# Kernel tuning notes

Hardware: AMD Instinct MI355X
Metric: run time of the kernel (lower is better)

The kernel has to match this reference:

```python
import jax, jax.numpy as jnp
import numpy as np

EPS = 1e-06


def setup_inputs() -> dict:
    key = jax.random.key(0)
    k1, k2 = jax.random.split(key)
    x = jax.random.normal(k1, (16, 64, 256, 256), dtype=jnp.float32)
    gamma = jax.random.normal(k2, (1,), dtype=jnp.float32)
    return {"x": x, "gamma": gamma}


def reference(x, gamma):
    B, C, H, W = x.shape
    N = H * W
    v = x.reshape(B, C, N)                      # Q = K = V = flattened x
    # l2_norm: normalize across channel dim (dim=-2) per spatial position
    inv_norm = 1.0 / (jnp.linalg.norm(v, axis=1) + 1e-06)   # [B, N]
    qn = v * inv_norm[:, None, :]               # [B, C, N], Q and K normalized identically
    q_sum = jnp.sum(qn, axis=1)                 # [B, N] (sum over channels)
    # tailor_sum: 1 / (N + K^T-summed-Q + eps) -> [B, C]
    tailor = 1.0 / (N + jnp.einsum('bcn,bn->bc', qn, q_sum) + EPS)
    value_sum = jnp.sum(v, axis=1)[:, None, :]  # [B, 1, N], broadcasts over C
    matrix = jnp.einsum('bcn,bmn->bcm', v, qn)  # V @ K^T : [B, C, C]
    matrix_sum = value_sum + jnp.einsum('bcm,bmn->bcn', matrix, qn)  # [B, C, N]
    weight_value = matrix_sum * tailor[:, :, None]
    return x + gamma * weight_value.reshape(B, C, H, W)
```

## Files before the change

kernel.cpp:

```cpp
#include <hip/hip_runtime.h>
#include <stdint.h>

#define BATCH 16
#define CDIM 64
#define NDIM 65536
#define EPSV 1e-6f

typedef __attribute__((ext_vector_type(8))) _Float16 f16x8;
typedef __attribute__((ext_vector_type(4))) float f32x4;
typedef __attribute__((ext_vector_type(4))) uint32_t u32x4;
typedef __attribute__((ext_vector_type(4))) short s16x4;

static __device__ __forceinline__ short h2s(_Float16 h) {
    return (short)__builtin_bit_cast(unsigned short, h);
}
static __device__ __forceinline__ _Float16 s2h(short s) {
    return __builtin_bit_cast(_Float16, (unsigned short)s);
}

#define T1 256
#define P1 264
#define CHUNKS 4
#define NTILE1 64

__global__ __launch_bounds__(256, 4)
void gram_kernel(const float* __restrict__ x, float* __restrict__ pmat,
                 float* __restrict__ pt, short* __restrict__ ut,
                 float2* __restrict__ meta) {
    __shared__ __align__(16) short ldsU[CDIM][P1];
    __shared__ __align__(16) float ldsG[T1];
    __shared__ float red[4][CDIM];

    const int tid = threadIdx.x;
    const int b = blockIdx.x >> 6;
    const int tileIdx = blockIdx.x & 63;
    const int w = tid >> 6;
    const int lane = tid & 63;
    const int cq = lane >> 4;
    const int cr = lane & 15;

    f32x4 acc0 = {0.f, 0.f, 0.f, 0.f};
    f32x4 acc1 = acc0, acc2 = acc0, acc3 = acc0;
    float tpart = 0.f;

    const float* xbase = x + (size_t)b * CDIM * NDIM;

    for (int chunk = 0; chunk < CHUNKS; ++chunk) {
        const int n0 = tileIdx * (T1 * CHUNKS) + chunk * T1;
        const int n = n0 + tid;
        const float* xb = xbase + n;
        float ss = 0.f, cs = 0.f;
#pragma unroll 8
        for (int c = 0; c < CDIM; ++c) {
            float v = __builtin_nontemporal_load(xb + (size_t)c * NDIM);
            ss += v * v;
            cs += v;
            ldsU[c][tid] = h2s((_Float16)v);
        }
        const float inv = 1.f / (sqrtf(ss) + EPSV);
        const float sq = sqrtf(inv);
        const _Float16 sqh = (_Float16)sq;
        ldsG[tid] = inv * sq * cs;
        meta[(size_t)b * NDIM + n] = make_float2(cs, (float)sqh);
        short* urow = ut + ((size_t)b * NDIM + n) * CDIM;
#pragma unroll
        for (int c8 = 0; c8 < CDIM; c8 += 8) {
            uint32_t pk0, pk1, pk2, pk3;
#pragma unroll
            for (int j = 0; j < 4; ++j) {
                _Float16 u0 = s2h(ldsU[c8 + 2 * j][tid]) * sqh;
                _Float16 u1 = s2h(ldsU[c8 + 2 * j + 1][tid]) * sqh;
                ldsU[c8 + 2 * j][tid] = h2s(u0);
                ldsU[c8 + 2 * j + 1][tid] = h2s(u1);
                uint32_t p = (uint32_t)__builtin_bit_cast(unsigned short, u0) |
                             ((uint32_t)__builtin_bit_cast(unsigned short, u1) << 16);
                if (j == 0) pk0 = p; else if (j == 1) pk1 = p;
                else if (j == 2) pk2 = p; else pk3 = p;
            }
            *(u32x4*)(urow + c8) = (u32x4){pk0, pk1, pk2, pk3};
        }
        __syncthreads();
#pragma unroll
        for (int ks = 0; ks < 8; ++ks) {
            const int k0 = ks * 32 + cq * 8;
            f16x8 afrag = *(const f16x8*)&ldsU[w * 16 + cr][k0];
            f16x8 b0 = *(const f16x8*)&ldsU[cr][k0];
            f16x8 b1 = *(const f16x8*)&ldsU[16 + cr][k0];
            f16x8 b2 = *(const f16x8*)&ldsU[32 + cr][k0];
            f16x8 b3 = *(const f16x8*)&ldsU[48 + cr][k0];
            acc0 = __builtin_amdgcn_mfma_f32_16x16x32_f16(afrag, b0, acc0, 0, 0, 0);
            acc1 = __builtin_amdgcn_mfma_f32_16x16x32_f16(afrag, b1, acc1, 0, 0, 0);
            acc2 = __builtin_amdgcn_mfma_f32_16x16x32_f16(afrag, b2, acc2, 0, 0, 0);
            acc3 = __builtin_amdgcn_mfma_f32_16x16x32_f16(afrag, b3, acc3, 0, 0, 0);
        }
#pragma unroll
        for (int i = 0; i < 8; ++i) {
            const int nb = w * 64 + i * 8;
            f16x8 uf = *(const f16x8*)&ldsU[lane][nb];
            f32x4 g0 = *(const f32x4*)&ldsG[nb];
            f32x4 g1 = *(const f32x4*)&ldsG[nb + 4];
#pragma unroll
            for (int j = 0; j < 4; ++j) {
                tpart += (float)uf[j] * g0[j];
                tpart += (float)uf[j + 4] * g1[j];
            }
        }
        __syncthreads();
    }
    red[w][lane] = tpart;
    __syncthreads();
    if (tid < CDIM) {
        pt[(size_t)blockIdx.x * CDIM + tid] =
            red[0][tid] + red[1][tid] + red[2][tid] + red[3][tid];
    }
    float* pm = pmat + (size_t)blockIdx.x * CDIM * CDIM;
    const f32x4 accs[4] = {acc0, acc1, acc2, acc3};
#pragma unroll
    for (int mt = 0; mt < 4; ++mt) {
#pragma unroll
        for (int r = 0; r < 4; ++r) {
            const int row = w * 16 + cq * 4 + r;
            const int col = mt * 16 + cr;
            pm[row * CDIM + col] = accs[mt][r];
        }
    }
}

__global__ __launch_bounds__(256, 4)
void reduce_kernel(const float* __restrict__ pmat, const float* __restrict__ pt,
                   short* __restrict__ matb, float* __restrict__ tl) {
    const int blk = blockIdx.x;
    const int tid = threadIdx.x;
    if (blk < 256) {
        const int b = blk >> 4;
        const int o = (blk & 15) * 256 + tid;
        float s = 0.f;
#pragma unroll 8
        for (int t = 0; t < NTILE1; ++t)
            s += __builtin_nontemporal_load(
                &pmat[((size_t)(b * NTILE1 + t)) * (CDIM * CDIM) + o]);
        matb[(size_t)b * CDIM * CDIM + o] = h2s((_Float16)s);
    } else {
        const int idx = (blk - 256) * 256 + tid;
        const int b = idx >> 6;
        const int c = idx & 63;
        float s = 0.f;
#pragma unroll 8
        for (int t = 0; t < NTILE1; ++t)
            s += __builtin_nontemporal_load(&pt[(size_t)(b * NTILE1 + t) * CDIM + c]);
        tl[idx] = 1.f / ((float)NDIM + s + EPSV);
    }
}

#define PM 72

__global__ __launch_bounds__(256, 3)
void out_kernel(const short* __restrict__ ut, const short* __restrict__ matb,
                const float* __restrict__ tl, const float2* __restrict__ meta,
                const float* __restrict__ gamma, float* __restrict__ out) {
    __shared__ __align__(16) short ldsM[CDIM][PM];
    __shared__ float ldsTL[CDIM];

    const int tid = threadIdx.x;
    const int bid = (int)(gridDim.x - 1 - blockIdx.x);
    const int b = bid >> 8;
    const int n0 = (bid & 255) * 256;
    const int w = tid >> 6;
    const int lane = tid & 63;
    const int cq = lane >> 4;
    const int cr = lane & 15;

    {
        const short* mb = matb + (size_t)b * CDIM * CDIM;
        const int c = tid >> 2;
        const int seg = (tid & 3) * 16;
        u32x4 q0 = *(const u32x4*)(mb + c * CDIM + seg);
        u32x4 q1 = *(const u32x4*)(mb + c * CDIM + seg + 8);
        *(u32x4*)&ldsM[c][seg] = q0;
        *(u32x4*)&ldsM[c][seg + 8] = q1;
    }
    if (tid < CDIM) ldsTL[tid] = tl[b * CDIM + tid];
    __syncthreads();

    f16x8 afrag[4][2];
#pragma unroll
    for (int ct = 0; ct < 4; ++ct)
#pragma unroll
        for (int ks = 0; ks < 2; ++ks)
            afrag[ct][ks] = *(const f16x8*)&ldsM[ct * 16 + cr][ks * 32 + cq * 8];

    f32x4 acc[4][4];
#pragma unroll
    for (int p = 0; p < 4; ++p)
#pragma unroll
        for (int ct = 0; ct < 4; ++ct)
            acc[p][ct] = (f32x4){0.f, 0.f, 0.f, 0.f};

    const short* ub = ut + (size_t)b * NDIM * CDIM;

#pragma unroll
    for (int p = 0; p < 4; ++p) {
        const int n = n0 + (w * 4 + p) * 16 + cr;
        const short* urow = ub + (size_t)n * CDIM;
#pragma unroll
        for (int ks = 0; ks < 2; ++ks) {
            f16x8 bfrag = *(const f16x8*)(urow + ks * 32 + cq * 8);
#pragma unroll
            for (int ct = 0; ct < 4; ++ct)
                acc[p][ct] = __builtin_amdgcn_mfma_f32_16x16x32_f16(
                    afrag[ct][ks], bfrag, acc[p][ct], 0, 0, 0);
        }
    }

    const float g = gamma[0];
    float* obase = out + (size_t)b * CDIM * NDIM;
#pragma unroll
    for (int p = 0; p < 4; ++p) {
        const int n = n0 + (w * 4 + p) * 16 + cr;
        const float2 ms = meta[(size_t)b * NDIM + n];
        const float csn = ms.x;
        const float sn = ms.y;
        const float rs = 1.0f / sn;
        const short* urow = ub + (size_t)n * CDIM;
#pragma unroll
        for (int ct = 0; ct < 4; ++ct) {
            const int c0 = ct * 16 + cq * 4;
            s16x4 uv = *(const s16x4*)(urow + c0);
#pragma unroll
            for (int r = 0; r < 4; ++r) {
                const int c = c0 + r;
                float val = (float)s2h(uv[r]) * rs +
                            g * ldsTL[c] * (csn + sn * acc[p][ct][r]);
                __builtin_nontemporal_store(val, obase + (size_t)c * NDIM + n);
            }
        }
    }
}

extern "C" void kernel_launch(void* const* d_in, const int* in_sizes, int n_in,
                              void* d_out, int out_size, void* d_ws, size_t ws_size,
                              hipStream_t stream) {
    const float* x = (const float*)d_in[0];
    const float* gamma = (const float*)d_in[1];
    float* out = (float*)d_out;
    float* ws = (float*)d_ws;
    short* ut = (short*)ws;
    float* pmat = ws + (size_t)33554432;
    float* pt = pmat + (size_t)1024 * CDIM * CDIM;
    float2* meta = (float2*)(pt + (size_t)1024 * CDIM);
    short* matb = (short*)((float*)meta + (size_t)2 * BATCH * NDIM);
    float* tl = (float*)(matb + (size_t)BATCH * CDIM * CDIM);

    hipLaunchKernelGGL(gram_kernel, dim3(BATCH * NTILE1), dim3(256), 0, stream,
                       x, pmat, pt, ut, meta);
    hipLaunchKernelGGL(reduce_kernel, dim3(260), dim3(256), 0, stream,
                       pmat, pt, matb, tl);
    hipLaunchKernelGGL(out_kernel, dim3(BATCH * 256), dim3(256), 0, stream,
                       ut, matb, tl, meta, gamma, out);
}
```

Measured before the change: 534.1 us.

## Store raw fp16 x, apply inverse norm in MFMA A-operand, compute tailor sum via MFMA

The gram kernel now stores unscaled fp16 x rows to the workspace and keeps the inverse norm separately. The 1/||v|| scaling is applied to only the A fragment inside the MFMA loop, which removes the sqrt-split rescaling pass over LDS. The per-channel tailor sum, previously a scalar dot-product loop plus a block reduction, is now an extra MFMA with a masked B operand. The output kernel reads raw x values and the stored inverse norm, and its launch bounds are raised to allow 4 blocks per SM. The trade-offs are 32 extra registers for packing, more fp16 rounding of inv and inv*cs, and wasted MFMA lanes for the tailor term.

New measurement: 590.6 us. +10.6%, slower.

```diff
diff --git a/kernel.cpp b/kernel.cpp
--- a/kernel.cpp
+++ b/kernel.cpp
@@ -16,6 +16,9 @@
 }
 static __device__ __forceinline__ _Float16 s2h(short s) {
     return __builtin_bit_cast(_Float16, (unsigned short)s);
+}
+static __device__ __forceinline__ unsigned short h2u(_Float16 h) {
+    return __builtin_bit_cast(unsigned short, h);
 }
 
 #define T1 256
@@ -28,8 +31,8 @@
                  float* __restrict__ pt, short* __restrict__ ut,
                  float2* __restrict__ meta) {
     __shared__ __align__(16) short ldsU[CDIM][P1];
-    __shared__ __align__(16) float ldsG[T1];
-    __shared__ float red[4][CDIM];
+    __shared__ __align__(16) unsigned short ldsI[T1];
+    __shared__ __align__(16) unsigned short ldsGk[T1];
 
     const int tid = threadIdx.x;
     const int b = blockIdx.x >> 6;
@@ -40,8 +43,7 @@
     const int cr = lane & 15;
 
     f32x4 acc0 = {0.f, 0.f, 0.f, 0.f};
-    f32x4 acc1 = acc0, acc2 = acc0, acc3 = acc0;
-    float tpart = 0.f;
+    f32x4 acc1 = acc0, acc2 = acc0, acc3 = acc0, acct = acc0;
 
     const float* xbase = x + (size_t)b * CDIM * NDIM;
 
@@ -50,68 +52,57 @@
         const int n = n0 + tid;
         const float* xb = xbase + n;
         float ss = 0.f, cs = 0.f;
-#pragma unroll 8
-        for (int c = 0; c < CDIM; ++c) {
-            float v = __builtin_nontemporal_load(xb + (size_t)c * NDIM);
-            ss += v * v;
-            cs += v;
-            ldsU[c][tid] = h2s((_Float16)v);
+        uint32_t r[32];
+#pragma unroll
+        for (int cp = 0; cp < 32; ++cp) {
+            float v0 = __builtin_nontemporal_load(xb + (size_t)(2 * cp) * NDIM);
+            float v1 = __builtin_nontemporal_load(xb + (size_t)(2 * cp + 1) * NDIM);
+            ss += v0 * v0;
+            ss += v1 * v1;
+            cs += v0 + v1;
+            _Float16 h0 = (_Float16)v0, h1 = (_Float16)v1;
+            ldsU[2 * cp][tid] = h2s(h0);
+            ldsU[2 * cp + 1][tid] = h2s(h1);
+            r[cp] = (uint32_t)h2u(h0) | ((uint32_t)h2u(h1) << 16);
         }
         const float inv = 1.f / (sqrtf(ss) + EPSV);
-        const float sq = sqrtf(inv);
-        const _Float16 sqh = (_Float16)sq;
-        ldsG[tid] = inv * sq * cs;
-        meta[(size_t)b * NDIM + n] = make_float2(cs, (float)sqh);
+        meta[(size_t)b * NDIM + n] = make_float2(cs, inv);
+        ldsI[tid] = h2u((_Float16)inv);
+        ldsGk[tid] = h2u((_Float16)(inv * cs));
         short* urow = ut + ((size_t)b * NDIM + n) * CDIM;
-#pragma unroll
-        for (int c8 = 0; c8 < CDIM; c8 += 8) {
-            uint32_t pk0, pk1, pk2, pk3;
-#pragma unroll
-            for (int j = 0; j < 4; ++j) {
-                _Float16 u0 = s2h(ldsU[c8 + 2 * j][tid]) * sqh;
-                _Float16 u1 = s2h(ldsU[c8 + 2 * j + 1][tid]) * sqh;
-                ldsU[c8 + 2 * j][tid] = h2s(u0);
-                ldsU[c8 + 2 * j + 1][tid] = h2s(u1);
-                uint32_t p = (uint32_t)__builtin_bit_cast(unsigned short, u0) |
-                             ((uint32_t)__builtin_bit_cast(unsigned short, u1) << 16);
-                if (j == 0) pk0 = p; else if (j == 1) pk1 = p;
-                else if (j == 2) pk2 = p; else pk3 = p;
-            }
-            *(u32x4*)(urow + c8) = (u32x4){pk0, pk1, pk2, pk3};
-        }
+        *(u32x4*)(urow)      = (u32x4){r[0], r[1], r[2], r[3]};
+        *(u32x4*)(urow + 8)  = (u32x4){r[4], r[5], r[6], r[7]};
+        *(u32x4*)(urow + 16) = (u32x4){r[8], r[9], r[10], r[11]};
+        *(u32x4*)(urow + 24) = (u32x4){r[12], r[13], r[14], r[15]};
+        *(u32x4*)(urow + 32) = (u32x4){r[16], r[17], r[18], r[19]};
+        *(u32x4*)(urow + 40) = (u32x4){r[20], r[21], r[22], r[23]};
+        *(u32x4*)(urow + 48) = (u32x4){r[24], r[25], r[26], r[27]};
+        *(u32x4*)(urow + 56) = (u32x4){r[28], r[29], r[30], r[31]};
         __syncthreads();
 #pragma unroll
         for (int ks = 0; ks < 8; ++ks) {
             const int k0 = ks * 32 + cq * 8;
-            f16x8 afrag = *(const f16x8*)&ldsU[w * 16 + cr][k0];
+            f16x8 araw = *(const f16x8*)&ldsU[w * 16 + cr][k0];
+            f16x8 ipk = *(const f16x8*)&ldsI[k0];
+            f16x8 ascl = araw * ipk;
             f16x8 b0 = *(const f16x8*)&ldsU[cr][k0];
             f16x8 b1 = *(const f16x8*)&ldsU[16 + cr][k0];
             f16x8 b2 = *(const f16x8*)&ldsU[32 + cr][k0];
             f16x8 b3 = *(const f16x8*)&ldsU[48 + cr][k0];
-            acc0 = __builtin_amdgcn_mfma_f32_16x16x32_f16(afrag, b0, acc0, 0, 0, 0);
-            acc1 = __builtin_amdgcn_mfma_f32_16x16x32_f16(afrag, b1, acc1, 0, 0, 0);
-            acc2 = __builtin_amdgcn_mfma_f32_16x16x32_f16(afrag, b2, acc2, 0, 0, 0);
-            acc3 = __builtin_amdgcn_mfma_f32_16x16x32_f16(afrag, b3, acc3, 0, 0, 0);
-        }
-#pragma unroll
-        for (int i = 0; i < 8; ++i) {
-            const int nb = w * 64 + i * 8;
-            f16x8 uf = *(const f16x8*)&ldsU[lane][nb];
-            f32x4 g0 = *(const f32x4*)&ldsG[nb];
-            f32x4 g1 = *(const f32x4*)&ldsG[nb + 4];
-#pragma unroll
-            for (int j = 0; j < 4; ++j) {
-                tpart += (float)uf[j] * g0[j];
-                tpart += (float)uf[j + 4] * g1[j];
-            }
+            acc0 = __builtin_amdgcn_mfma_f32_16x16x32_f16(ascl, b0, acc0, 0, 0, 0);
+            acc1 = __builtin_amdgcn_mfma_f32_16x16x32_f16(ascl, b1, acc1, 0, 0, 0);
+            acc2 = __builtin_amdgcn_mfma_f32_16x16x32_f16(ascl, b2, acc2, 0, 0, 0);
+            acc3 = __builtin_amdgcn_mfma_f32_16x16x32_f16(ascl, b3, acc3, 0, 0, 0);
+            f16x8 gk = *(const f16x8*)&ldsGk[k0];
+            f16x8 bt = (cr == 0) ? gk : (f16x8)(_Float16)0.f;
+            acct = __builtin_amdgcn_mfma_f32_16x16x32_f16(ascl, bt, acct, 0, 0, 0);
         }
         __syncthreads();
     }
-    red[w][lane] = tpart;
-    __syncthreads();
-    if (tid < CDIM) {
-        pt[(size_t)blockIdx.x * CDIM + tid] =
-            red[0][tid] + red[1][tid] + red[2][tid] + red[3][tid];
+    if (cr == 0) {
+        float* ptb = pt + (size_t)blockIdx.x * CDIM + w * 16 + cq * 4;
+#pragma unroll
+        for (int r = 0; r < 4; ++r) ptb[r] = acct[r];
     }
     float* pm = pmat + (size_t)blockIdx.x * CDIM * CDIM;
     const f32x4 accs[4] = {acc0, acc1, acc2, acc3};
@@ -154,7 +145,7 @@
 
 #define PM 72
 
-__global__ __launch_bounds__(256, 3)
+__global__ __launch_bounds__(256, 4)
 void out_kernel(const short* __restrict__ ut, const short* __restrict__ matb,
                 const float* __restrict__ tl, const float2* __restrict__ meta,
                 const float* __restrict__ gamma, float* __restrict__ out) {
@@ -219,8 +210,7 @@
         const int n = n0 + (w * 4 + p) * 16 + cr;
         const float2 ms = meta[(size_t)b * NDIM + n];
         const float csn = ms.x;
-        const float sn = ms.y;
-        const float rs = 1.0f / sn;
+        const float invn = ms.y;
         const short* urow = ub + (size_t)n * CDIM;
 #pragma unroll
         for (int ct = 0; ct < 4; ++ct) {
@@ -229,8 +219,8 @@
 #pragma unroll
             for (int r = 0; r < 4; ++r) {
                 const int c = c0 + r;
-                float val = (float)s2h(uv[r]) * rs +
-                            g * ldsTL[c] * (csn + sn * acc[p][ct][r]);
+                float val = (float)s2h(uv[r]) +
+                            g * ldsTL[c] * (csn + invn * acc[p][ct][r]);
                 __builtin_nontemporal_store(val, obase + (size_t)c * NDIM + n);
             }
         }
```
